# Optimization experiments

Measured on AMD Instinct MI355X. Metric: run time of the kernel, lower is better.

The kernel has to match this reference:

```python
import jax, jax.numpy as jnp
import numpy as np

HEADS = 8
DIM_HEAD = 64
SCALE = DIM_HEAD ** -0.5
EPS = 1e-5


def layernorm(t, g, b):
    mu = t.mean(-1, keepdims=True)
    var = ((t - mu) ** 2).mean(-1, keepdims=True)
    return (t - mu) * jax.lax.rsqrt(var + EPS) * g + b


def setup_inputs() -> dict:
    key = jax.random.key(0)
    ks = jax.random.split(key, 12)
    b, n, dim, inner = 2, 2048, 512, HEADS * DIM_HEAD
    s = dim ** -0.5
    return {
        "x": jax.random.normal(ks[0], (b, n, dim), jnp.float32),
        "context": jax.random.normal(ks[1], (b, n, dim), jnp.float32),
        "g_x": jnp.ones((dim,), jnp.float32),
        "b_x": jnp.zeros((dim,), jnp.float32),
        "g_c": jnp.ones((dim,), jnp.float32),
        "b_c": jnp.zeros((dim,), jnp.float32),
        "W_qk": jax.random.normal(ks[2], (dim, inner), jnp.float32) * s,
        "W_cqk": jax.random.normal(ks[3], (dim, inner), jnp.float32) * s,
        "W_v": jax.random.normal(ks[4], (dim, inner), jnp.float32) * s,
        "W_cv": jax.random.normal(ks[5], (dim, inner), jnp.float32) * s,
        "W_out": jax.random.normal(ks[6], (inner, dim), jnp.float32) * s,
        "b_out": jnp.zeros((dim,), jnp.float32),
        "W_cout": jax.random.normal(ks[7], (inner, dim), jnp.float32) * s,
        "b_cout": jnp.zeros((dim,), jnp.float32),
    }


def reference(x, context, g_x, b_x, g_c, b_c, W_qk, W_cqk, W_v, W_cv, W_out, b_out, W_cout, b_cout):
    b, i, _ = x.shape
    j = context.shape[1]
    xn = layernorm(x, g_x, b_x)
    cn = layernorm(context, g_c, b_c)

    def split_heads(t):  # [b, n, h*d] -> [b, h, n, d]
        return t.reshape(t.shape[0], t.shape[1], HEADS, DIM_HEAD).transpose(0, 2, 1, 3)

    qk = split_heads(xn @ W_qk)
    cqk = split_heads(cn @ W_cqk)
    v = split_heads(xn @ W_v)
    cv = split_heads(cn @ W_cv)

    sim = jnp.einsum('bhid,bhjd->bhij', qk, cqk) * SCALE  # [b,h,i,j]
    attn = jax.nn.softmax(sim, axis=-1)           # rows: x attends to context
    context_attn = jax.nn.softmax(sim, axis=-2)   # cols: context attends to x

    out = jnp.einsum('bhij,bhjd->bhid', attn, cv)            # [b,h,i,d]
    context_out = jnp.einsum('bhij,bhid->bhjd', context_attn, v)  # [b,h,j,d]

    def merge_heads(t):  # [b,h,n,d] -> [b,n,h*d]
        return t.transpose(0, 2, 1, 3).reshape(t.shape[0], t.shape[2], HEADS * DIM_HEAD)

    out = merge_heads(out) @ W_out + b_out
    context_out = merge_heads(context_out) @ W_cout + b_cout
    return out, context_out
```

## Files before the change

### kernel.cpp

```cpp
#include <hip/hip_runtime.h>


typedef _Float16 half_t;
typedef __attribute__((ext_vector_type(2))) _Float16 half2v;
typedef __attribute__((ext_vector_type(4))) _Float16 half4v;
typedef __attribute__((ext_vector_type(8))) _Float16 half8v;
typedef __attribute__((ext_vector_type(4))) float floatx4;

#define MFMA16(a, b, c) __builtin_amdgcn_mfma_f32_16x16x32_f16((a), (b), (c), 0, 0, 0)

#if defined(__has_builtin)
#if __has_builtin(__builtin_amdgcn_exp2f)
#define EXP2F(x) __builtin_amdgcn_exp2f(x)
#else
#define EXP2F(x) exp2f(x)
#endif
#else
#define EXP2F(x) exp2f(x)
#endif

__device__ __forceinline__ half2v pk2(float a, float b) {
#if defined(__has_builtin) && __has_builtin(__builtin_amdgcn_cvt_pkrtz)
    union { __fp16 __attribute__((ext_vector_type(2))) i; half2v o; } u;
    u.i = __builtin_amdgcn_cvt_pkrtz(a, b);
    return u.o;
#else
    half2v r; r[0] = (half_t)a; r[1] = (half_t)b; return r;
#endif
}

__device__ __forceinline__ void gld16(const half_t* g, half_t* l) {
    __builtin_amdgcn_global_load_lds(
        (const __attribute__((address_space(1))) void*)g,
        (__attribute__((address_space(3))) void*)l, 16, 0, 0);
}

__global__ __launch_bounds__(256) void prep_kernel(
    const float* __restrict__ x, const float* __restrict__ ctx,
    const float* __restrict__ gx, const float* __restrict__ bx,
    const float* __restrict__ gc, const float* __restrict__ bc,
    half_t* __restrict__ xn, half_t* __restrict__ cn,
    const float* __restrict__ W0, const float* __restrict__ W1,
    const float* __restrict__ W2, const float* __restrict__ W3,
    const float* __restrict__ W4, const float* __restrict__ W5,
    half_t* __restrict__ Wt)
{
    __shared__ alignas(16) half_t Ts[128][136];
    const int blk = blockIdx.x;
    const int tid = threadIdx.x;
    const int wave = tid >> 6, lane = tid & 63;

    if (blk < 2048) {
        const int row = blk * 4 + wave;
        const float *src, *g, *b;
        half_t* dst;
        if (row < 4096) {
            src = x + (size_t)row * 512; g = gx; b = bx; dst = xn + (size_t)row * 512;
        } else {
            const size_t r = (size_t)(row - 4096);
            src = ctx + r * 512; g = gc; b = bc; dst = cn + r * 512;
        }
        const float4 a0 = *(const float4*)(src + lane * 4);
        const float4 a1 = *(const float4*)(src + 256 + lane * 4);
        float s = a0.x + a0.y + a0.z + a0.w + a1.x + a1.y + a1.z + a1.w;
        float q = a0.x * a0.x + a0.y * a0.y + a0.z * a0.z + a0.w * a0.w +
                  a1.x * a1.x + a1.y * a1.y + a1.z * a1.z + a1.w * a1.w;
#pragma unroll
        for (int m = 1; m < 64; m <<= 1) {
            s += __shfl_xor(s, m);
            q += __shfl_xor(q, m);
        }
        const float mean = s * (1.0f / 512.0f);
        const float var = q * (1.0f / 512.0f) - mean * mean;
        const float rs = rsqrtf(var + 1e-5f);
        const float4 g0 = *(const float4*)(g + lane * 4);
        const float4 g1 = *(const float4*)(g + 256 + lane * 4);
        const float4 b0 = *(const float4*)(b + lane * 4);
        const float4 b1 = *(const float4*)(b + 256 + lane * 4);
        half4v h0, h1;
        h0[0] = (half_t)((a0.x - mean) * rs * g0.x + b0.x);
        h0[1] = (half_t)((a0.y - mean) * rs * g0.y + b0.y);
        h0[2] = (half_t)((a0.z - mean) * rs * g0.z + b0.z);
        h0[3] = (half_t)((a0.w - mean) * rs * g0.w + b0.w);
        h1[0] = (half_t)((a1.x - mean) * rs * g1.x + b1.x);
        h1[1] = (half_t)((a1.y - mean) * rs * g1.y + b1.y);
        h1[2] = (half_t)((a1.z - mean) * rs * g1.z + b1.z);
        h1[3] = (half_t)((a1.w - mean) * rs * g1.w + b1.w);
        *(half4v*)(dst + lane * 4) = h0;
        *(half4v*)(dst + 256 + lane * 4) = h1;
        return;
    }

    const int b2 = blk - 2048;
    const int mat = b2 >> 4, tile = b2 & 15;
    const float* src;
    switch (mat) {
        case 0: src = W0; break;
        case 1: src = W1; break;
        case 2: src = W2; break;
        case 3: src = W3; break;
        case 4: src = W4; break;
        default: src = W5; break;
    }
    const int tr0 = (tile >> 2) * 128;
    const int tc0 = (tile & 3) * 128;
#pragma unroll
    for (int p = 0; p < 16; ++p) {
        const int idx = p * 256 + tid;
        const int r = idx >> 5, c4 = (idx & 31) * 4;
        const float4 w = *(const float4*)(src + (size_t)(tr0 + r) * 512 + tc0 + c4);
        Ts[c4 + 0][r] = (half_t)w.x;
        Ts[c4 + 1][r] = (half_t)w.y;
        Ts[c4 + 2][r] = (half_t)w.z;
        Ts[c4 + 3][r] = (half_t)w.w;
    }
    __syncthreads();
    half_t* dst = Wt + (size_t)mat * 262144;
#pragma unroll
    for (int p = 0; p < 8; ++p) {
        const int idx = p * 256 + tid;
        const int row = idx >> 4, ch = (idx & 15) * 8;
        *(half8v*)(dst + (size_t)(tc0 + row) * 512 + tr0 + ch) = *(const half8v*)&Ts[row][ch];
    }
}

__global__ __launch_bounds__(256) void gemm_in_kernel(
    const half_t* __restrict__ xn, const half_t* __restrict__ cn,
    const half_t* __restrict__ Wt,
    half_t* __restrict__ qk, half_t* __restrict__ v_t,
    half_t* __restrict__ cqk, half_t* __restrict__ cv_t)
{
    const half_t* A; const half_t* B; half_t* O;
    switch (blockIdx.z) {
        case 0:  A = xn; B = Wt;          O = qk;   break;
        case 1:  A = xn; B = Wt + 262144; O = v_t;  break;
        case 2:  A = cn; B = Wt + 524288; O = cqk;  break;
        default: A = cn; B = Wt + 786432; O = cv_t; break;
    }
    const int tr = blockIdx.z & 1;
    const int mt0 = blockIdx.x * 128;
    const int nt0 = blockIdx.y * 128;

    __shared__ alignas(16) half_t As[128 * 64];
    __shared__ alignas(16) half_t Ws[128 * 64];

    const int tid = threadIdx.x;
    const int wave = tid >> 6, lane = tid & 63;
    const int wr = wave >> 1, wc = wave & 1;
    const int q4 = lane >> 4, c = lane & 15;

    int srow[4], scol[4];
#pragma unroll
    for (int p = 0; p < 4; ++p) {
        const int ofs = p * 4096 + wave * 1024 + lane * 16;
        const int row = ofs >> 7;
        const int pc = (ofs >> 4) & 7;
        srow[p] = row;
        scol[p] = (pc ^ (row & 7)) * 8;
    }

    const half_t* P1 = tr ? As : Ws;
    const half_t* P2 = tr ? Ws : As;

    const floatx4 z4 = {0.f, 0.f, 0.f, 0.f};
    floatx4 acc[4][4];
#pragma unroll
    for (int mt = 0; mt < 4; ++mt)
#pragma unroll
        for (int nt = 0; nt < 4; ++nt) acc[mt][nt] = z4;

    for (int kb = 0; kb < 8; ++kb) {
        const int k0 = kb * 64;
#pragma unroll
        for (int p = 0; p < 4; ++p) {
            const int lofs = p * 2048 + wave * 512;
            gld16(A + (size_t)(mt0 + srow[p]) * 512 + k0 + scol[p], As + lofs);
            gld16(B + (size_t)(nt0 + srow[p]) * 512 + k0 + scol[p], Ws + lofs);
        }
        __syncthreads();
#pragma unroll
        for (int kt = 0; kt < 2; ++kt) {
            half8v f1[4], f2[4];
#pragma unroll
            for (int i = 0; i < 4; ++i) {
                const int r1 = wr * 64 + i * 16 + c;
                const int r2 = wc * 64 + i * 16 + c;
                f1[i] = *(const half8v*)&P1[(r1 << 6) + (((kt * 4 + q4) ^ (r1 & 7)) << 3)];
                f2[i] = *(const half8v*)&P2[(r2 << 6) + (((kt * 4 + q4) ^ (r2 & 7)) << 3)];
            }
#pragma unroll
            for (int mt = 0; mt < 4; ++mt)
#pragma unroll
                for (int nt = 0; nt < 4; ++nt)
                    acc[mt][nt] = MFMA16(f1[mt], f2[nt], acc[mt][nt]);
        }
        __syncthreads();
    }

    const int bb = mt0 >> 11;
    const int nnb = mt0 & 2047;
    if (tr) {
#pragma unroll
        for (int mt = 0; mt < 4; ++mt) {
            const int row = nnb + wr * 64 + mt * 16 + q4 * 4;
#pragma unroll
            for (int nt = 0; nt < 4; ++nt) {
                const int col = nt0 + wc * 64 + nt * 16 + c;
                const int h = col >> 6, dd = col & 63;
                half4v pk;
                pk[0] = (half_t)acc[mt][nt][0];
                pk[1] = (half_t)acc[mt][nt][1];
                pk[2] = (half_t)acc[mt][nt][2];
                pk[3] = (half_t)acc[mt][nt][3];
                *(half4v*)(O + ((size_t)(bb * 8 + h) * 64 + dd) * 2048 + row) = pk;
            }
        }
    } else {
#pragma unroll
        for (int mt = 0; mt < 4; ++mt) {
            const int colw = nt0 + wr * 64 + mt * 16 + q4 * 4;
            const int h = colw >> 6, dd = colw & 63;
#pragma unroll
            for (int nt = 0; nt < 4; ++nt) {
                const int row = nnb + wc * 64 + nt * 16 + c;
                half4v pk;
                pk[0] = (half_t)acc[mt][nt][0];
                pk[1] = (half_t)acc[mt][nt][1];
                pk[2] = (half_t)acc[mt][nt][2];
                pk[3] = (half_t)acc[mt][nt][3];
                *(half4v*)(O + ((size_t)(bb * 8 + h) * 2048 + row) * 64 + dd) = pk;
            }
        }
    }
}

__global__ __launch_bounds__(256, 4) void flash_kernel(
    const half_t* __restrict__ qk, const half_t* __restrict__ cqk,
    const half_t* __restrict__ v_t, const half_t* __restrict__ cv_t,
    float* __restrict__ Pbuf, float* __restrict__ Lbuf)
{
    const int bh = blockIdx.x, it = blockIdx.y;
    const int dir = blockIdx.z >> 1, js = blockIdx.z & 1;
    const half_t* Q  = dir ? cqk : qk;
    const half_t* K  = dir ? qk  : cqk;
    const half_t* VT = dir ? v_t : cv_t;
    const half_t* Qb = Q + (size_t)bh * (2048 * 64);
    const half_t* Kb = K + (size_t)bh * (2048 * 64);
    const half_t* VTb = VT + (size_t)bh * (64 * 2048);
    float* Pb = Pbuf + (size_t)((js * 2 + dir) * 16 + bh) * (2048 * 64);
    float* Lb = Lbuf + (size_t)((js * 2 + dir) * 16 + bh) * 2048;

    __shared__ alignas(16) half_t Ks[128 * 64];
    __shared__ alignas(16) half_t CVs[64 * 128];

    const int tid = threadIdx.x;
    const int wave = tid >> 6, lane = tid & 63;
    const int q4 = lane >> 4, c = lane & 15;

    half8v onesb;
#pragma unroll
    for (int j = 0; j < 8; ++j) onesb[j] = (c == 0) ? (half_t)1.0f : (half_t)0.0f;

    half8v qf[2][2];
#pragma unroll
    for (int mt = 0; mt < 2; ++mt)
#pragma unroll
        for (int kt = 0; kt < 2; ++kt) {
            half8v v = *(const half8v*)(Qb + (size_t)(it * 128 + wave * 32 + mt * 16 + c) * 64 +
                                        kt * 32 + q4 * 8);
            qf[mt][kt] = v * (half_t)0.18033688f;
        }

    const floatx4 z4 = {0.f, 0.f, 0.f, 0.f};
    floatx4 accT[4][2];
    floatx4 accL[2];
#pragma unroll
    for (int vt = 0; vt < 4; ++vt)
#pragma unroll
        for (int mt = 0; mt < 2; ++mt) accT[vt][mt] = z4;
    accL[0] = z4; accL[1] = z4;

    const int jt0 = js * 8;
    for (int jt = jt0; jt < jt0 + 8; ++jt) {
        const half_t* Kt = Kb + (size_t)jt * 8192;
        const half_t* Vt = VTb + jt * 128;
        __syncthreads();
#pragma unroll
        for (int p = 0; p < 4; ++p) {
            const int base = p * 256 + wave * 64;
            const int cidx = base + lane;
            const int krow = cidx >> 3, kch = cidx & 7;
            const int ksw = ((krow >> 2) ^ (krow & 3)) & 7;
            gld16(Kt + (size_t)krow * 64 + ((kch ^ ksw) * 8), Ks + base * 8);
            const int vrow = cidx >> 4, vch = cidx & 15;
            gld16(Vt + (size_t)vrow * 2048 + ((vch ^ (vrow & 15)) * 8), CVs + base * 8);
        }
        __syncthreads();

#pragma unroll
        for (int g = 0; g < 4; ++g) {
            floatx4 st[2][2];
#pragma unroll
            for (int t = 0; t < 2; ++t) {
                const int jr = g * 32 + t * 4 + ((c >> 2) << 3) + (c & 3);
                const int sw = ((jr >> 2) ^ (jr & 3)) & 7;
                const half8v kf0 = *(const half8v*)&Ks[jr * 64 + ((q4 ^ sw) * 8)];
                const half8v kf1 = *(const half8v*)&Ks[jr * 64 + (((4 + q4) ^ sw) * 8)];
#pragma unroll
                for (int mt = 0; mt < 2; ++mt) {
                    floatx4 tt = MFMA16(kf0, qf[mt][0], z4);
                    st[mt][t] = MFMA16(kf1, qf[mt][1], tt);
                }
            }
            half8v pf[2];
#pragma unroll
            for (int mt = 0; mt < 2; ++mt) {
                union { half8v v; half2v h2[4]; } u;
                u.h2[0] = pk2(EXP2F(fminf(st[mt][0][0], 15.0f)),
                              EXP2F(fminf(st[mt][0][1], 15.0f)));
                u.h2[1] = pk2(EXP2F(fminf(st[mt][0][2], 15.0f)),
                              EXP2F(fminf(st[mt][0][3], 15.0f)));
                u.h2[2] = pk2(EXP2F(fminf(st[mt][1][0], 15.0f)),
                              EXP2F(fminf(st[mt][1][1], 15.0f)));
                u.h2[3] = pk2(EXP2F(fminf(st[mt][1][2], 15.0f)),
                              EXP2F(fminf(st[mt][1][3], 15.0f)));
                pf[mt] = u.v;
            }
#pragma unroll
            for (int vt = 0; vt < 4; ++vt) {
                const half8v bf = *(const half8v*)&CVs[(vt * 16 + c) * 128 +
                                                       (((g * 4 + q4) ^ c) * 8)];
#pragma unroll
                for (int mt = 0; mt < 2; ++mt)
                    accT[vt][mt] = MFMA16(bf, pf[mt], accT[vt][mt]);
            }
#pragma unroll
            for (int mt = 0; mt < 2; ++mt)
                accL[mt] = MFMA16(onesb, pf[mt], accL[mt]);
        }
    }

#pragma unroll
    for (int mt = 0; mt < 2; ++mt) {
        const int row = it * 128 + wave * 32 + mt * 16 + c;
        if (q4 == 0) Lb[row] = accL[mt][0];
#pragma unroll
        for (int vt = 0; vt < 4; ++vt) {
            float4 o;
            o.x = accT[vt][mt][0];
            o.y = accT[vt][mt][1];
            o.z = accT[vt][mt][2];
            o.w = accT[vt][mt][3];
            *(float4*)(Pb + (size_t)row * 64 + vt * 16 + q4 * 4) = o;
        }
    }
}

__global__ __launch_bounds__(256) void combine_kernel(
    const float* __restrict__ Pbuf, const float* __restrict__ Lbuf,
    half_t* __restrict__ out_h, half_t* __restrict__ ctx_out_h)
{
    const int tid = threadIdx.x;
    const int rg = blockIdx.x * 16 + (tid >> 4);
    const int q = tid & 15;
    const int i = rg & 2047;
    const int bh = (rg >> 11) & 15;
    const int dir = rg >> 15;

    const size_t pb0 = (size_t)(dir * 16 + bh) * (2048 * 64) + (size_t)i * 64 + q * 4;
    const size_t pb1 = pb0 + (size_t)2 * 16 * 2048 * 64;
    const float4 a0 = *(const float4*)(Pbuf + pb0);
    const float4 a1 = *(const float4*)(Pbuf + pb1);
    const size_t lb0 = (size_t)(dir * 16 + bh) * 2048 + i;
    const float l = Lbuf[lb0] + Lbuf[lb0 + (size_t)2 * 16 * 2048];
    const float rl = 1.0f / l;

    half_t* Out = dir ? ctx_out_h : out_h;
    half4v pk;
    pk[0] = (half_t)((a0.x + a1.x) * rl);
    pk[1] = (half_t)((a0.y + a1.y) * rl);
    pk[2] = (half_t)((a0.z + a1.z) * rl);
    pk[3] = (half_t)((a0.w + a1.w) * rl);
    *(half4v*)(Out + (size_t)(bh >> 3) * 2048 * 512 + (size_t)i * 512 +
               (bh & 7) * 64 + q * 4) = pk;
}

__global__ __launch_bounds__(256) void gemm_out_kernel(
    const half_t* __restrict__ out_h, const half_t* __restrict__ ctx_out_h,
    const half_t* __restrict__ Wt,
    const float* __restrict__ bout, const float* __restrict__ bcout,
    float* __restrict__ dout)
{
    const half_t* A; const half_t* B; const float* bias; float* O;
    if (blockIdx.z == 0) { A = out_h;     B = Wt + 1048576; bias = bout;  O = dout; }
    else                 { A = ctx_out_h; B = Wt + 1310720; bias = bcout; O = dout + 2097152; }

    const int mt0 = blockIdx.x * 64;
    const int nt0 = blockIdx.y * 128;

    __shared__ alignas(16) half_t As[64 * 64];
    __shared__ alignas(16) half_t Ws[128 * 64];

    const int tid = threadIdx.x;
    const int wave = tid >> 6, lane = tid & 63;
    const int wr = wave >> 1, wc = wave & 1;
    const int q4 = lane >> 4, c = lane & 15;

    int srow[4], scol[4];
#pragma unroll
    for (int p = 0; p < 4; ++p) {
        const int ofs = p * 4096 + wave * 1024 + lane * 16;
        const int row = ofs >> 7;
        const int pc = (ofs >> 4) & 7;
        srow[p] = row;
        scol[p] = (pc ^ (row & 7)) * 8;
    }

    const floatx4 z4 = {0.f, 0.f, 0.f, 0.f};
    floatx4 acc[4][2];
#pragma unroll
    for (int mt = 0; mt < 4; ++mt)
#pragma unroll
        for (int nt = 0; nt < 2; ++nt) acc[mt][nt] = z4;

    for (int kb = 0; kb < 8; ++kb) {
        const int k0 = kb * 64;
#pragma unroll
        for (int p = 0; p < 4; ++p) {
            const int lofs = p * 2048 + wave * 512;
            gld16(B + (size_t)(nt0 + srow[p]) * 512 + k0 + scol[p], Ws + lofs);
            if (p < 2)
                gld16(A + (size_t)(mt0 + srow[p]) * 512 + k0 + scol[p], As + lofs);
        }
        __syncthreads();
#pragma unroll
        for (int kt = 0; kt < 2; ++kt) {
            half8v f1[4], f2[2];
#pragma unroll
            for (int i = 0; i < 4; ++i) {
                const int r1 = wr * 64 + i * 16 + c;
                f1[i] = *(const half8v*)&Ws[(r1 << 6) + (((kt * 4 + q4) ^ (r1 & 7)) << 3)];
            }
#pragma unroll
            for (int i = 0; i < 2; ++i) {
                const int r2 = wc * 32 + i * 16 + c;
                f2[i] = *(const half8v*)&As[(r2 << 6) + (((kt * 4 + q4) ^ (r2 & 7)) << 3)];
            }
#pragma unroll
            for (int mt = 0; mt < 4; ++mt)
#pragma unroll
                for (int nt = 0; nt < 2; ++nt)
                    acc[mt][nt] = MFMA16(f1[mt], f2[nt], acc[mt][nt]);
        }
        __syncthreads();
    }

#pragma unroll
    for (int mt = 0; mt < 4; ++mt) {
        const int col = nt0 + wr * 64 + mt * 16 + q4 * 4;
        const float4 bv = *(const float4*)(bias + col);
#pragma unroll
        for (int nt = 0; nt < 2; ++nt) {
            const int row = mt0 + wc * 32 + nt * 16 + c;
            float4 o;
            o.x = acc[mt][nt][0] + bv.x;
            o.y = acc[mt][nt][1] + bv.y;
            o.z = acc[mt][nt][2] + bv.z;
            o.w = acc[mt][nt][3] + bv.w;
            *(float4*)(O + (size_t)row * 512 + col) = o;
        }
    }
}

extern "C" void kernel_launch(void* const* d_in, const int* in_sizes, int n_in,
                              void* d_out, int out_size, void* d_ws, size_t ws_size,
                              hipStream_t stream)
{
    (void)in_sizes; (void)n_in; (void)out_size; (void)ws_size;
    const float* x      = (const float*)d_in[0];
    const float* ctx    = (const float*)d_in[1];
    const float* g_x    = (const float*)d_in[2];
    const float* b_x    = (const float*)d_in[3];
    const float* g_c    = (const float*)d_in[4];
    const float* b_c    = (const float*)d_in[5];
    const float* W_qk   = (const float*)d_in[6];
    const float* W_cqk  = (const float*)d_in[7];
    const float* W_v    = (const float*)d_in[8];
    const float* W_cv   = (const float*)d_in[9];
    const float* W_out  = (const float*)d_in[10];
    const float* b_out  = (const float*)d_in[11];
    const float* W_cout = (const float*)d_in[12];
    const float* b_cout = (const float*)d_in[13];
    float* out = (float*)d_out;

    half_t* ws = (half_t*)d_ws;
    const size_t SEG = 2097152;
    half_t* xn        = ws;
    half_t* cn        = ws + 1 * SEG;
    half_t* qk        = ws + 2 * SEG;
    half_t* cqk       = ws + 3 * SEG;
    half_t* v_t       = ws + 4 * SEG;
    half_t* cv_t      = ws + 5 * SEG;
    half_t* Wt        = ws + 6 * SEG;
    half_t* out_h     = xn;
    half_t* ctx_out_h = cn;
    float* Pbuf = (float*)(ws + 6 * SEG + 1572864);
    float* Lbuf = Pbuf + (size_t)2 * 2 * 16 * 2048 * 64;

    prep_kernel<<<2144, 256, 0, stream>>>(x, ctx, g_x, b_x, g_c, b_c, xn, cn,
                                          W_qk, W_v, W_cqk, W_cv, W_out, W_cout, Wt);
    gemm_in_kernel<<<dim3(32, 4, 4), 256, 0, stream>>>(xn, cn, Wt, qk, v_t, cqk, cv_t);
    flash_kernel<<<dim3(16, 16, 4), 256, 0, stream>>>(qk, cqk, v_t, cv_t, Pbuf, Lbuf);
    combine_kernel<<<4096, 256, 0, stream>>>(Pbuf, Lbuf, out_h, ctx_out_h);
    gemm_out_kernel<<<dim3(64, 4, 2), 256, 0, stream>>>(out_h, ctx_out_h, Wt, b_out, b_cout, out);
}
```

Baseline: 177.4 us.

## Double-buffer K/V tiles, double rows per wave, sum row normalizer in VALU

Flash kernel now double-buffers the K and transposed-V shared-memory tiles so the next tile's global loads are issued while the current tile is computed, with one barrier per iteration. Each wave processes 64 query rows instead of 32, halving the grid and reusing each K/V fragment across twice as many MFMAs. The row-sum normalizer is now accumulated with scalar adds plus cross-lane shuffles instead of an extra MFMA against a ones vector. Shared memory doubles, register pressure rises (launch bounds lowered to 2 blocks per SM), and fewer blocks reduce occupancy and grid fill.

```diff
diff --git a/kernel.cpp b/kernel.cpp
--- a/kernel.cpp
+++ b/kernel.cpp
@@ -234,7 +234,23 @@
     }
 }
 
-__global__ __launch_bounds__(256, 4) void flash_kernel(
+__device__ __forceinline__ void stage_tile(const half_t* Kt, const half_t* Vt,
+                                           half_t* ksb, half_t* cvb,
+                                           int wave, int lane)
+{
+#pragma unroll
+    for (int p = 0; p < 4; ++p) {
+        const int base = p * 256 + wave * 64;
+        const int cidx = base + lane;
+        const int krow = cidx >> 3, kch = cidx & 7;
+        const int ksw = ((krow >> 2) ^ (krow & 3)) & 7;
+        gld16(Kt + (size_t)krow * 64 + ((kch ^ ksw) * 8), ksb + base * 8);
+        const int vrow = cidx >> 4, vch = cidx & 15;
+        gld16(Vt + (size_t)vrow * 2048 + ((vch ^ (vrow & 15)) * 8), cvb + base * 8);
+    }
+}
+
+__global__ __launch_bounds__(256, 2) void flash_kernel(
     const half_t* __restrict__ qk, const half_t* __restrict__ cqk,
     const half_t* __restrict__ v_t, const half_t* __restrict__ cv_t,
     float* __restrict__ Pbuf, float* __restrict__ Lbuf)
@@ -250,100 +266,99 @@
     float* Pb = Pbuf + (size_t)((js * 2 + dir) * 16 + bh) * (2048 * 64);
     float* Lb = Lbuf + (size_t)((js * 2 + dir) * 16 + bh) * 2048;
 
-    __shared__ alignas(16) half_t Ks[128 * 64];
-    __shared__ alignas(16) half_t CVs[64 * 128];
+    __shared__ alignas(16) half_t Ks[2][128 * 64];
+    __shared__ alignas(16) half_t CVs[2][64 * 128];
 
     const int tid = threadIdx.x;
     const int wave = tid >> 6, lane = tid & 63;
     const int q4 = lane >> 4, c = lane & 15;
 
-    half8v onesb;
-#pragma unroll
-    for (int j = 0; j < 8; ++j) onesb[j] = (c == 0) ? (half_t)1.0f : (half_t)0.0f;
-
-    half8v qf[2][2];
-#pragma unroll
-    for (int mt = 0; mt < 2; ++mt)
+    half8v qf[4][2];
+#pragma unroll
+    for (int mt = 0; mt < 4; ++mt)
 #pragma unroll
         for (int kt = 0; kt < 2; ++kt) {
-            half8v v = *(const half8v*)(Qb + (size_t)(it * 128 + wave * 32 + mt * 16 + c) * 64 +
+            half8v v = *(const half8v*)(Qb + (size_t)(it * 256 + wave * 64 + mt * 16 + c) * 64 +
                                         kt * 32 + q4 * 8);
             qf[mt][kt] = v * (half_t)0.18033688f;
         }
 
     const floatx4 z4 = {0.f, 0.f, 0.f, 0.f};
-    floatx4 accT[4][2];
-    floatx4 accL[2];
+    floatx4 accT[4][4];
+    float accLf[4];
 #pragma unroll
     for (int vt = 0; vt < 4; ++vt)
 #pragma unroll
-        for (int mt = 0; mt < 2; ++mt) accT[vt][mt] = z4;
-    accL[0] = z4; accL[1] = z4;
+        for (int mt = 0; mt < 4; ++mt) accT[vt][mt] = z4;
+#pragma unroll
+    for (int mt = 0; mt < 4; ++mt) accLf[mt] = 0.f;
 
     const int jt0 = js * 8;
-    for (int jt = jt0; jt < jt0 + 8; ++jt) {
-        const half_t* Kt = Kb + (size_t)jt * 8192;
-        const half_t* Vt = VTb + jt * 128;
-        __syncthreads();
-#pragma unroll
-        for (int p = 0; p < 4; ++p) {
-            const int base = p * 256 + wave * 64;
-            const int cidx = base + lane;
-            const int krow = cidx >> 3, kch = cidx & 7;
-            const int ksw = ((krow >> 2) ^ (krow & 3)) & 7;
-            gld16(Kt + (size_t)krow * 64 + ((kch ^ ksw) * 8), Ks + base * 8);
-            const int vrow = cidx >> 4, vch = cidx & 15;
-            gld16(Vt + (size_t)vrow * 2048 + ((vch ^ (vrow & 15)) * 8), CVs + base * 8);
-        }
-        __syncthreads();
+    stage_tile(Kb + (size_t)jt0 * 8192, VTb + jt0 * 128, Ks[0], CVs[0], wave, lane);
+    __syncthreads();
+
+    for (int n = 0; n < 8; ++n) {
+        const int jt = jt0 + n;
+        const int cur = n & 1;
+        if (n < 7)
+            stage_tile(Kb + (size_t)(jt + 1) * 8192, VTb + (size_t)(jt + 1) * 128,
+                       Ks[cur ^ 1], CVs[cur ^ 1], wave, lane);
+        const half_t* ks = Ks[cur];
+        const half_t* cv = CVs[cur];
 
 #pragma unroll
         for (int g = 0; g < 4; ++g) {
-            floatx4 st[2][2];
+            floatx4 st[4][2];
 #pragma unroll
             for (int t = 0; t < 2; ++t) {
                 const int jr = g * 32 + t * 4 + ((c >> 2) << 3) + (c & 3);
                 const int sw = ((jr >> 2) ^ (jr & 3)) & 7;
-                const half8v kf0 = *(const half8v*)&Ks[jr * 64 + ((q4 ^ sw) * 8)];
-                const half8v kf1 = *(const half8v*)&Ks[jr * 64 + (((4 + q4) ^ sw) * 8)];
-#pragma unroll
-                for (int mt = 0; mt < 2; ++mt) {
+                const half8v kf0 = *(const half8v*)&ks[jr * 64 + ((q4 ^ sw) * 8)];
+                const half8v kf1 = *(const half8v*)&ks[jr * 64 + (((4 + q4) ^ sw) * 8)];
+#pragma unroll
+                for (int mt = 0; mt < 4; ++mt) {
                     floatx4 tt = MFMA16(kf0, qf[mt][0], z4);
                     st[mt][t] = MFMA16(kf1, qf[mt][1], tt);
                 }
             }
-            half8v pf[2];
-#pragma unroll
-            for (int mt = 0; mt < 2; ++mt) {
+            half8v pf[4];
+#pragma unroll
+            for (int mt = 0; mt < 4; ++mt) {
+                const float e0 = EXP2F(fminf(st[mt][0][0], 15.0f));
+                const float e1 = EXP2F(fminf(st[mt][0][1], 15.0f));
+                const float e2 = EXP2F(fminf(st[mt][0][2], 15.0f));
+                const float e3 = EXP2F(fminf(st[mt][0][3], 15.0f));
+                const float e4 = EXP2F(fminf(st[mt][1][0], 15.0f));
+                const float e5 = EXP2F(fminf(st[mt][1][1], 15.0f));
+                const float e6 = EXP2F(fminf(st[mt][1][2], 15.0f));
+                const float e7 = EXP2F(fminf(st[mt][1][3], 15.0f));
+                accLf[mt] += ((e0 + e1) + (e2 + e3)) + ((e4 + e5) + (e6 + e7));
                 union { half8v v; half2v h2[4]; } u;
-                u.h2[0] = pk2(EXP2F(fminf(st[mt][0][0], 15.0f)),
-                              EXP2F(fminf(st[mt][0][1], 15.0f)));
-                u.h2[1] = pk2(EXP2F(fminf(st[mt][0][2], 15.0f)),
-                              EXP2F(fminf(st[mt][0][3], 15.0f)));
-                u.h2[2] = pk2(EXP2F(fminf(st[mt][1][0], 15.0f)),
-                              EXP2F(fminf(st[mt][1][1], 15.0f)));
-                u.h2[3] = pk2(EXP2F(fminf(st[mt][1][2], 15.0f)),
-                              EXP2F(fminf(st[mt][1][3], 15.0f)));
+                u.h2[0] = pk2(e0, e1);
+                u.h2[1] = pk2(e2, e3);
+                u.h2[2] = pk2(e4, e5);
+                u.h2[3] = pk2(e6, e7);
                 pf[mt] = u.v;
             }
 #pragma unroll
             for (int vt = 0; vt < 4; ++vt) {
-                const half8v bf = *(const half8v*)&CVs[(vt * 16 + c) * 128 +
-                                                       (((g * 4 + q4) ^ c) * 8)];
-#pragma unroll
-                for (int mt = 0; mt < 2; ++mt)
+                const half8v bf = *(const half8v*)&cv[(vt * 16 + c) * 128 +
+                                                     (((g * 4 + q4) ^ c) * 8)];
+#pragma unroll
+                for (int mt = 0; mt < 4; ++mt)
                     accT[vt][mt] = MFMA16(bf, pf[mt], accT[vt][mt]);
             }
-#pragma unroll
-            for (int mt = 0; mt < 2; ++mt)
-                accL[mt] = MFMA16(onesb, pf[mt], accL[mt]);
-        }
-    }
-
-#pragma unroll
-    for (int mt = 0; mt < 2; ++mt) {
-        const int row = it * 128 + wave * 32 + mt * 16 + c;
-        if (q4 == 0) Lb[row] = accL[mt][0];
+        }
+        __syncthreads();
+    }
+
+#pragma unroll
+    for (int mt = 0; mt < 4; ++mt) {
+        float l = accLf[mt];
+        l += __shfl_xor(l, 16);
+        l += __shfl_xor(l, 32);
+        const int row = it * 256 + wave * 64 + mt * 16 + c;
+        if (q4 == 0) Lb[row] = l;
 #pragma unroll
         for (int vt = 0; vt < 4; ++vt) {
             float4 o;
@@ -510,7 +525,7 @@
     prep_kernel<<<2144, 256, 0, stream>>>(x, ctx, g_x, b_x, g_c, b_c, xn, cn,
                                           W_qk, W_v, W_cqk, W_cv, W_out, W_cout, Wt);
     gemm_in_kernel<<<dim3(32, 4, 4), 256, 0, stream>>>(xn, cn, Wt, qk, v_t, cqk, cv_t);
-    flash_kernel<<<dim3(16, 16, 4), 256, 0, stream>>>(qk, cqk, v_t, cv_t, Pbuf, Lbuf);
+    flash_kernel<<<dim3(16, 8, 4), 256, 0, stream>>>(qk, cqk, v_t, cv_t, Pbuf, Lbuf);
     combine_kernel<<<4096, 256, 0, stream>>>(Pbuf, Lbuf, out_h, ctx_out_h);
     gemm_out_kernel<<<dim3(64, 4, 2), 256, 0, stream>>>(out_h, ctx_out_h, Wt, b_out, b_cout, out);
 }
```

After: 259.6 us. 1.46x slower.
